# Kernel tuning notes

Measured on AMD Instinct MI355X. Metric: run time of the kernel, lower is better.

Reference implementation:

```python
import jax, jax.numpy as jnp
import numpy as np

THETA = 10000.0
NUM_HEADS = 16


def _rope(x, pos, theta):
    # x: [..., T, d_k], pos: [T]
    d_k = x.shape[-1]
    inv_freq = 1.0 / theta ** (jnp.arange(0, d_k, 2, dtype=jnp.float32) / d_k)
    ang = pos.astype(jnp.float32)[:, None] * inv_freq  # [T, d_k/2]
    cos, sin = jnp.cos(ang), jnp.sin(ang)
    x1, x2 = x[..., ::2], x[..., 1::2]
    even = x1 * cos - x2 * sin
    odd = x1 * sin + x2 * cos
    return jnp.stack([even, odd], axis=-1).reshape(x.shape)


def setup_inputs() -> dict:
    key = jax.random.key(0)
    ks = jax.random.split(key, 5)
    B, T, D = 4, 2048, 1024
    return {
        "in_features": jax.random.normal(ks[0], (B, T, D), dtype=jnp.float32),
        "token_positions": jnp.arange(T, dtype=jnp.int64 if jax.config.jax_enable_x64 else jnp.int32),
        "Wq": jax.random.normal(ks[1], (D, D), dtype=jnp.float32) * 0.02,
        "Wk": jax.random.normal(ks[2], (D, D), dtype=jnp.float32) * 0.02,
        "Wv": jax.random.normal(ks[3], (D, D), dtype=jnp.float32) * 0.02,
        "Wo": jax.random.normal(ks[4], (D, D), dtype=jnp.float32) * 0.02,
    }


def reference(in_features, token_positions, Wq, Wk, Wv, Wo):
    B, T, D = in_features.shape
    h = NUM_HEADS
    d_k = D // h
    # projections (weight stored [out, in], torch applies x @ W.T)
    Q = in_features @ Wq.T
    K = in_features @ Wk.T
    V = in_features @ Wv.T
    # [B, T, h*d_k] -> [B, h, T, d_k]
    Q = Q.reshape(B, T, h, d_k).transpose(0, 2, 1, 3)
    K = K.reshape(B, T, h, d_k).transpose(0, 2, 1, 3)
    V = V.reshape(B, T, h, d_k).transpose(0, 2, 1, 3)
    Q = _rope(Q, token_positions, THETA)
    K = _rope(K, token_positions, THETA)
    scores = jnp.einsum("bhqd,bhkd->bhqk", Q, K) / jnp.sqrt(jnp.float32(d_k))
    causal = jnp.tril(jnp.ones((T, T), dtype=bool))
    scores = jnp.where(causal, scores, -jnp.inf)
    attn = jax.nn.softmax(scores, axis=-1)
    heads = jnp.einsum("bhqk,bhkd->bhqd", attn, V)
    out = heads.transpose(0, 2, 1, 3).reshape(B, T, D)
    return out @ Wo.T
```

## Files before the change

### kernel.cpp

```cpp
#include <hip/hip_runtime.h>


typedef unsigned short u16;
typedef short short8 __attribute__((ext_vector_type(8)));
typedef float f32x4 __attribute__((ext_vector_type(4)));

#if defined(__has_builtin)
#if __has_builtin(__builtin_amdgcn_exp2f)
#define EXP2(x) __builtin_amdgcn_exp2f(x)
#else
#define EXP2(x) exp2f(x)
#endif
#else
#define EXP2(x) exp2f(x)
#endif

#define QSCALE 0.18033688011112042f
#define NEG_L2T_32 -0.4152410118609203f

__device__ __forceinline__ float bf2f(u16 u) {
  return __uint_as_float(((unsigned int)u) << 16);
}
__device__ __forceinline__ u16 f2bf(float f) {
  unsigned int x = __float_as_uint(f);
  x += 0x7fff + ((x >> 16) & 1);
  return (u16)(x >> 16);
}

__device__ __forceinline__ void glds16(const u16* g, u16* l) {
  __builtin_amdgcn_global_load_lds(
      (const __attribute__((address_space(1))) unsigned int*)g,
      (__attribute__((address_space(3))) unsigned int*)l, 16, 0, 0);
}

__global__ __launch_bounds__(256) void cvt_all(
    const float* __restrict__ X, const float* __restrict__ Wq,
    const float* __restrict__ Wk, const float* __restrict__ Wv,
    const float* __restrict__ Wo, u16* __restrict__ Xb,
    u16* __restrict__ Wqkvb, u16* __restrict__ Wob) {
  const int gid = blockIdx.x * 256 + threadIdx.x;
  const int i = gid * 8;
  const int M1 = 1 << 20;
  const float* src;
  u16* dst;
  int off;
  if (i < 8 * M1)        { src = X;  dst = Xb;            off = 0; }
  else if (i < 9 * M1)   { src = Wq; dst = Wqkvb;         off = 8 * M1; }
  else if (i < 10 * M1)  { src = Wk; dst = Wqkvb + M1;    off = 9 * M1; }
  else if (i < 11 * M1)  { src = Wv; dst = Wqkvb + 2*M1;  off = 10 * M1; }
  else                   { src = Wo; dst = Wob;           off = 11 * M1; }
  const int j = i - off;
  const float4 a = *(const float4*)(src + j);
  const float4 b = *(const float4*)(src + j + 4);
  short8 o;
  o[0] = (short)f2bf(a.x); o[1] = (short)f2bf(a.y);
  o[2] = (short)f2bf(a.z); o[3] = (short)f2bf(a.w);
  o[4] = (short)f2bf(b.x); o[5] = (short)f2bf(b.y);
  o[6] = (short)f2bf(b.z); o[7] = (short)f2bf(b.w);
  *(short8*)(dst + j) = o;
}

__global__ __launch_bounds__(256) void gemm_qkv(const u16* __restrict__ A,
                                                const u16* __restrict__ W,
                                                const int* __restrict__ pos,
                                                u16* __restrict__ Qr,
                                                u16* __restrict__ Kr,
                                                u16* __restrict__ Vd) {
  const int K = 1024;
  __shared__ __align__(16) u16 As[128 * 64];
  __shared__ __align__(16) u16 Bs[128 * 64];
  const int tid = threadIdx.x;
  const int m0 = blockIdx.y << 7;
  const int n0 = blockIdx.x << 7;
  const int w = tid >> 6, L = tid & 63;
  const int wm = (w >> 1) << 6, wn = (w & 1) << 6;
  const int lane15 = L & 15, quad = L >> 4;

  f32x4 acc[4][4] = {};

  const u16* Ap[4]; const u16* Bp[4];
  u16* Al[4]; u16* Bl[4];
#pragma unroll
  for (int i = 0; i < 4; ++i) {
    const int s = tid + (i << 8);
    const int row = s >> 3;
    const int c = ((s & 7) ^ (row & 7)) << 3;
    Ap[i] = A + (size_t)(m0 + row) * K + c;
    Bp[i] = W + (size_t)(n0 + row) * K + c;
    Al[i] = &As[s * 8];
    Bl[i] = &Bs[s * 8];
  }

  int offA[4][2], offB[4][2];
#pragma unroll
  for (int mt = 0; mt < 4; ++mt) {
    const int ra = wm + mt * 16 + lane15;
    const int rb = wn + mt * 16 + lane15;
    offA[mt][0] = ra * 64 + ((quad ^ (ra & 7)) << 3);
    offA[mt][1] = ra * 64 + (((quad + 4) ^ (ra & 7)) << 3);
    offB[mt][0] = rb * 64 + ((quad ^ (rb & 7)) << 3);
    offB[mt][1] = rb * 64 + (((quad + 4) ^ (rb & 7)) << 3);
  }

  for (int k0 = 0; k0 < K; k0 += 64) {
    __syncthreads();
#pragma unroll
    for (int i = 0; i < 4; ++i) glds16(Ap[i] + k0, Al[i]);
#pragma unroll
    for (int i = 0; i < 4; ++i) glds16(Bp[i] + k0, Bl[i]);
    __syncthreads();
#pragma unroll
    for (int ks = 0; ks < 2; ++ks) {
      short8 a[4], b[4];
#pragma unroll
      for (int mt = 0; mt < 4; ++mt) a[mt] = *(const short8*)&As[offA[mt][ks]];
#pragma unroll
      for (int nt = 0; nt < 4; ++nt) b[nt] = *(const short8*)&Bs[offB[nt][ks]];
#pragma unroll
      for (int mt = 0; mt < 4; ++mt)
#pragma unroll
        for (int nt = 0; nt < 4; ++nt)
          acc[mt][nt] =
              __builtin_amdgcn_mfma_f32_16x16x32_bf16(a[mt], b[nt], acc[mt][nt], 0, 0, 0);
    }
  }

  const int sel = n0 >> 10;
  const int ncol0 = (n0 & 1023) + wn;
  if (sel == 2) {
#pragma unroll
    for (int mt = 0; mt < 4; ++mt) {
      const int rbase = m0 + wm + mt * 16 + (quad << 2);
#pragma unroll
      for (int nt = 0; nt < 4; ++nt) {
        const int col = ncol0 + nt * 16 + lane15;
#pragma unroll
        for (int r = 0; r < 4; ++r)
          Vd[(size_t)(rbase + r) * 1024 + col] = f2bf(acc[mt][nt][r]);
      }
    }
  } else {
    u16* dst = sel ? Kr : Qr;
    const float sc = sel ? 1.0f : QSCALE;
    float invf[4];
#pragma unroll
    for (int nt = 0; nt < 4; ++nt) {
      const int d2 = ((ncol0 + nt * 16 + lane15) & 63) >> 1;
      invf[nt] = EXP2((float)d2 * NEG_L2T_32);
    }
#pragma unroll
    for (int mt = 0; mt < 4; ++mt) {
      const int rbase = m0 + wm + mt * 16 + (quad << 2);
#pragma unroll
      for (int r = 0; r < 4; ++r) {
        const int m = rbase + r;
        const int bb = m >> 11, tt = m & 2047;
        const float posf = (float)pos[tt];
#pragma unroll
        for (int nt = 0; nt < 4; ++nt) {
          const int col = ncol0 + nt * 16 + lane15;
          const int h = col >> 6, dcol = col & 63;
          float sn, cn;
          __sincosf(posf * invf[nt], &sn, &cn);
          const float self = acc[mt][nt][r];
          const float part = __shfl_xor(self, 1, 64);
          const float res = (dcol & 1) ? (part * sn + self * cn)
                                       : (self * cn - part * sn);
          dst[(((size_t)((bb * 16 + h) * 2048 + tt)) << 6) + dcol] = f2bf(res * sc);
        }
      }
    }
  }
}

__global__ __launch_bounds__(256) void gemm_bt(const u16* __restrict__ A,
                                               const u16* __restrict__ B,
                                               float* __restrict__ C,
                                               int M, int N, int K) {
  __shared__ __align__(16) u16 As[64 * 32];
  __shared__ __align__(16) u16 Bs[128 * 32];
  const int tid = threadIdx.x;
  const int m0 = blockIdx.y << 6;
  const int n0 = blockIdx.x << 7;
  const int w = tid >> 6, L = tid & 63;
  const int wm = (w >> 1) << 5, wn = (w & 1) << 6;
  const int lane15 = L & 15, quad = L >> 4;
  const int koff = quad << 3;

  f32x4 acc[2][4] = {};

  const int s0 = tid, s1 = tid + 256;
  const u16* A0 = A + (size_t)(m0 + (s0 >> 2)) * K + ((s0 & 3) << 3);
  const u16* B0 = B + (size_t)(n0 + (s0 >> 2)) * K + ((s0 & 3) << 3);
  const u16* B1 = B + (size_t)(n0 + (s1 >> 2)) * K + ((s1 & 3) << 3);
  u16* asd0 = &As[s0 * 8];
  u16* bsd0 = &Bs[s0 * 8]; u16* bsd1 = &Bs[s1 * 8];

  for (int k0 = 0; k0 < K; k0 += 32) {
    __syncthreads();
    glds16(A0 + k0, asd0);
    glds16(B0 + k0, bsd0);
    glds16(B1 + k0, bsd1);
    __syncthreads();
    short8 a[2], b[4];
#pragma unroll
    for (int mt = 0; mt < 2; ++mt)
      a[mt] = *(const short8*)&As[(wm + mt * 16 + lane15) * 32 + koff];
#pragma unroll
    for (int nt = 0; nt < 4; ++nt)
      b[nt] = *(const short8*)&Bs[(wn + nt * 16 + lane15) * 32 + koff];
#pragma unroll
    for (int mt = 0; mt < 2; ++mt)
#pragma unroll
      for (int nt = 0; nt < 4; ++nt)
        acc[mt][nt] =
            __builtin_amdgcn_mfma_f32_16x16x32_bf16(a[mt], b[nt], acc[mt][nt], 0, 0, 0);
  }

#pragma unroll
  for (int mt = 0; mt < 2; ++mt) {
    const int rbase = m0 + wm + mt * 16 + (quad << 2);
#pragma unroll
    for (int nt = 0; nt < 4; ++nt) {
      const int col = n0 + wn + nt * 16 + lane15;
#pragma unroll
      for (int r = 0; r < 4; ++r)
        C[(size_t)(rbase + r) * N + col] = acc[mt][nt][r];
    }
  }
}

__global__ __launch_bounds__(256) void transpose_v(const u16* __restrict__ Vlin,
                                                   u16* __restrict__ Vt) {
  __shared__ __align__(16) u16 tile[64][68];
  const int tid = threadIdx.x;
  const int bh = blockIdx.y, b = bh >> 4, h = bh & 15;
  const int t0 = blockIdx.x << 6;
#pragma unroll
  for (int i = 0; i < 4; ++i) {
    int s = tid + (i << 8);
    int tl = s >> 4, c4 = (s & 15) << 2;
    *(uint2*)&tile[tl][c4] =
        *(const uint2*)(Vlin + (((size_t)(b * 2048 + t0 + tl)) << 10) + (h << 6) + c4);
  }
  __syncthreads();
#pragma unroll
  for (int i = 0; i < 4; ++i) {
    int s = tid + (i << 8);
    int d = s >> 4, t4 = (s & 15) << 2;
    uint2 o;
    o.x = (unsigned)tile[t4 + 0][d] | ((unsigned)tile[t4 + 1][d] << 16);
    o.y = (unsigned)tile[t4 + 2][d] | ((unsigned)tile[t4 + 3][d] << 16);
    *(uint2*)(Vt + (((size_t)(bh * 64 + d)) << 11) + t0 + t4) = o;
  }
}

__global__ __launch_bounds__(256) void flash_attn(const u16* __restrict__ Q,
                                                  const u16* __restrict__ Kk,
                                                  const u16* __restrict__ Vt,
                                                  u16* __restrict__ O) {
  __shared__ __align__(16) u16 Ksm[64 * 72];
  __shared__ __align__(16) u16 Vsm[64 * 72];
  __shared__ __align__(16) u16 Psm[8][16 * 64];
  const int tid = threadIdx.x;
  const int w = tid >> 6, L = tid & 63;
  const int lane15 = L & 15, quad = L >> 4;
  const int g = blockIdx.x >> 6;
  const int bh = blockIdx.x & 63;
  const int b = bh >> 4, h = bh & 15;
  const int rq = lane15 >> 2;

  const int s0 = tid, s1 = tid + 256;
  const u16* kbase = Kk + ((size_t)bh << 17);
  const u16* kp0 = kbase + s0 * 8;
  const u16* kp1 = kbase + s1 * 8;
  const u16* vbase = Vt + ((size_t)bh << 17);
  const u16* vp0 = vbase + (size_t)(s0 >> 3) * 2048 + (s0 & 7) * 8;
  const u16* vp1 = vbase + (size_t)(s1 >> 3) * 2048 + (s1 & 7) * 8;
  const int d0 = (s0 >> 3) * 72 + (s0 & 7) * 8;
  const int d1 = (s1 >> 3) * 72 + (s1 & 7) * 8;

  for (int pass = 0; pass < 2; ++pass) {
    const int qt = pass ? (15 - g) : g;
    const int nkt = 2 * qt + 2;

    const size_t qrow = (size_t)bh * 2048 + qt * 128 + w * 32;
    short8 qa[2][2];
#pragma unroll
    for (int hf = 0; hf < 2; ++hf) {
      const size_t qb = (qrow + hf * 16 + lane15) << 6;
      qa[hf][0] = *(const short8*)(Q + qb + (quad << 3));
      qa[hf][1] = *(const short8*)(Q + qb + 32 + (quad << 3));
    }

    uint4 kr0 = *(const uint4*)kp0;
    uint4 kr1 = *(const uint4*)kp1;
    uint4 vr0 = *(const uint4*)vp0;
    uint4 vr1 = *(const uint4*)vp1;
    __syncthreads();
    *(uint4*)&Ksm[d0] = kr0; *(uint4*)&Ksm[d1] = kr1;
    *(uint4*)&Vsm[d0] = vr0; *(uint4*)&Vsm[d1] = vr1;
    __syncthreads();

    f32x4 o_acc[2][4] = {};
    float l_part[2][4] = {};
    const int B0w = qt * 128 + w * 32;

    for (int kt = 0; kt < nkt; ++kt) {
      if (kt + 1 < nkt) {
        kr0 = *(const uint4*)(kp0 + (size_t)(kt + 1) * 4096);
        kr1 = *(const uint4*)(kp1 + (size_t)(kt + 1) * 4096);
        vr0 = *(const uint4*)(vp0 + (kt + 1) * 64);
        vr1 = *(const uint4*)(vp1 + (kt + 1) * 64);
      }

      short8 kb[4][2];
#pragma unroll
      for (int nt = 0; nt < 4; ++nt) {
        kb[nt][0] = *(const short8*)&Ksm[(nt * 16 + lane15) * 72 + (quad << 3)];
        kb[nt][1] = *(const short8*)&Ksm[(nt * 16 + lane15) * 72 + 32 + (quad << 3)];
      }

      const bool act0 = (kt * 64 <= B0w + 15);
      const bool act1 = (kt * 64 <= B0w + 31);

#pragma unroll
      for (int hf = 0; hf < 2; ++hf) {
        const int B0 = B0w + hf * 16;
        if (kt * 64 > B0 + 15) continue;
        u16* pw = Psm[w * 2 + hf];

        f32x4 sc[4];
#pragma unroll
        for (int nt = 0; nt < 4; ++nt) {
          f32x4 a = {};
          a = __builtin_amdgcn_mfma_f32_16x16x32_bf16(qa[hf][0], kb[nt][0], a, 0, 0, 0);
          a = __builtin_amdgcn_mfma_f32_16x16x32_bf16(qa[hf][1], kb[nt][1], a, 0, 0, 0);
          sc[nt] = a;
        }

        if (kt * 64 + 63 > B0) {
#pragma unroll
          for (int nt = 0; nt < 4; ++nt)
#pragma unroll
            for (int r = 0; r < 4; ++r) {
              const int row = B0 + (quad << 2) + r;
              const int key = kt * 64 + nt * 16 + lane15;
              if (key > row) sc[nt][r] = -1e30f;
            }
        }

#pragma unroll
        for (int nt = 0; nt < 4; ++nt) {
          const int colsw = ((nt ^ quad) << 4) + lane15;
#pragma unroll
          for (int r = 0; r < 4; ++r) {
            const float p = EXP2(sc[nt][r]);
            l_part[hf][r] += p;
            pw[((quad << 2) + r) * 64 + colsw] = (u16)(__float_as_uint(p) >> 16);
          }
        }
      }
      asm volatile("" ::: "memory");

      short8 pa[2][2];
      if (act0) {
#pragma unroll
        for (int ks = 0; ks < 2; ++ks)
          pa[0][ks] = *(const short8*)&Psm[w * 2][lane15 * 64 +
                                               ((ks * 32 + quad * 8) ^ (rq << 4))];
      }
      if (act1) {
#pragma unroll
        for (int ks = 0; ks < 2; ++ks)
          pa[1][ks] = *(const short8*)&Psm[w * 2 + 1][lane15 * 64 +
                                               ((ks * 32 + quad * 8) ^ (rq << 4))];
      }
#pragma unroll
      for (int ks = 0; ks < 2; ++ks) {
#pragma unroll
        for (int dt = 0; dt < 4; ++dt) {
          const short8 vb =
              *(const short8*)&Vsm[(dt * 16 + lane15) * 72 + ks * 32 + quad * 8];
          if (act0)
            o_acc[0][dt] =
                __builtin_amdgcn_mfma_f32_16x16x32_bf16(pa[0][ks], vb, o_acc[0][dt], 0, 0, 0);
          if (act1)
            o_acc[1][dt] =
                __builtin_amdgcn_mfma_f32_16x16x32_bf16(pa[1][ks], vb, o_acc[1][dt], 0, 0, 0);
        }
      }

      if (kt + 1 < nkt) {
        __syncthreads();
        *(uint4*)&Ksm[d0] = kr0; *(uint4*)&Ksm[d1] = kr1;
        *(uint4*)&Vsm[d0] = vr0; *(uint4*)&Vsm[d1] = vr1;
        __syncthreads();
      }
    }

#pragma unroll
    for (int hf = 0; hf < 2; ++hf) {
#pragma unroll
      for (int r = 0; r < 4; ++r) {
        float l = l_part[hf][r];
#pragma unroll
        for (int off = 1; off < 16; off <<= 1) l += __shfl_xor(l, off, 64);
        const float inv = 1.f / l;
        const int t = qt * 128 + w * 32 + hf * 16 + (quad << 2) + r;
        const size_t obase = (((size_t)b * 2048 + t) << 10) + (h << 6);
#pragma unroll
        for (int dt = 0; dt < 4; ++dt)
          O[obase + dt * 16 + lane15] = f2bf(o_acc[hf][dt][r] * inv);
      }
    }
  }
}

extern "C" void kernel_launch(void* const* d_in, const int* in_sizes, int n_in,
                              void* d_out, int out_size, void* d_ws, size_t ws_size,
                              hipStream_t stream) {
  const float* X  = (const float*)d_in[0];
  const int* pos  = (const int*)d_in[1];
  const float* Wq = (const float*)d_in[2];
  const float* Wk = (const float*)d_in[3];
  const float* Wv = (const float*)d_in[4];
  const float* Wo = (const float*)d_in[5];
  float* out = (float*)d_out;

  char* ws = (char*)d_ws;
  const size_t SZ = (size_t)8192 * 1024 * sizeof(u16);
  const size_t WSZ = (size_t)1024 * 1024 * sizeof(u16);
  u16* Vlin = (u16*)(ws + 0 * SZ);
  u16* Qr   = (u16*)(ws + 1 * SZ);
  u16* Kr   = (u16*)(ws + 2 * SZ);
  u16* Vt   = (u16*)(ws + 3 * SZ);
  u16* Xb   = (u16*)(ws + 4 * SZ);
  u16* Oh   = Vlin;
  char* wtail = ws + 5 * SZ;
  u16* Wqkvb = (u16*)(wtail);
  u16* Wob   = (u16*)(wtail + 3 * WSZ);

  const dim3 blk(256);

  cvt_all<<<6144, blk, 0, stream>>>(X, Wq, Wk, Wv, Wo, Xb, Wqkvb, Wob);
  gemm_qkv<<<dim3(24, 64), blk, 0, stream>>>(Xb, Wqkvb, pos, Qr, Kr, Vlin);
  transpose_v<<<dim3(32, 64), blk, 0, stream>>>(Vlin, Vt);
  flash_attn<<<512, blk, 0, stream>>>(Qr, Kr, Vt, Oh);
  gemm_bt<<<dim3(8, 128), blk, 0, stream>>>(Oh, Wob, out, 8192, 1024, 1024);
}
```

Before: 271.4 us.

## Fuse V transpose into QKV GEMM, double-buffer attention K/V, widen output GEMM K-tile

The QKV GEMM epilogue for V tiles now stages the accumulator through shared memory with a swizzle and writes V directly in transposed [b,h,d,t] layout, so the separate transpose kernel and its round trip through global memory go away. Flash attention double-buffers its K/V shared tiles, which drops one barrier per iteration. The output projection GEMM moves to a 64-wide K tile with XOR-swizzled LDS addressing, halving the number of loop iterations and barriers. The cost is more shared memory per block, which may lower occupancy, plus an extra sync in the QKV epilogue.

```diff
diff --git a/kernel.cpp b/kernel.cpp
--- a/kernel.cpp
+++ b/kernel.cpp
@@ -25,6 +25,9 @@
   unsigned int x = __float_as_uint(f);
   x += 0x7fff + ((x >> 16) & 1);
   return (u16)(x >> 16);
+}
+__device__ __forceinline__ unsigned int pack2(float x, float y) {
+  return (unsigned int)f2bf(x) | ((unsigned int)f2bf(y) << 16);
 }
 
 __device__ __forceinline__ void glds16(const u16* g, u16* l) {
@@ -65,10 +68,11 @@
                                                 const int* __restrict__ pos,
                                                 u16* __restrict__ Qr,
                                                 u16* __restrict__ Kr,
-                                                u16* __restrict__ Vd) {
+                                                u16* __restrict__ Vt) {
   const int K = 1024;
-  __shared__ __align__(16) u16 As[128 * 64];
-  __shared__ __align__(16) u16 Bs[128 * 64];
+  __shared__ __align__(16) u16 SM[16384];
+  u16* As = SM;
+  u16* Bs = SM + 8192;
   const int tid = threadIdx.x;
   const int m0 = blockIdx.y << 7;
   const int n0 = blockIdx.x << 7;
@@ -126,18 +130,34 @@
   }
 
   const int sel = n0 >> 10;
-  const int ncol0 = (n0 & 1023) + wn;
+  const int ncol0w = (n0 & 1023) + wn;
   if (sel == 2) {
+    const int b = m0 >> 11, t0 = m0 & 2047;
+    const int h0 = (n0 & 1023) >> 6;
+    __syncthreads();
 #pragma unroll
     for (int mt = 0; mt < 4; ++mt) {
-      const int rbase = m0 + wm + mt * 16 + (quad << 2);
+      const int tb = wm + mt * 16 + (quad << 2);
 #pragma unroll
       for (int nt = 0; nt < 4; ++nt) {
-        const int col = ncol0 + nt * 16 + lane15;
-#pragma unroll
-        for (int r = 0; r < 4; ++r)
-          Vd[(size_t)(rbase + r) * 1024 + col] = f2bf(acc[mt][nt][r]);
-      }
+        const int dp = wn + nt * 16 + lane15;
+        const int e = dp * 128 + ((tb & ~7) ^ ((dp & 15) << 3)) + (tb & 7);
+        uint2 v;
+        v.x = pack2(acc[mt][nt][0], acc[mt][nt][1]);
+        v.y = pack2(acc[mt][nt][2], acc[mt][nt][3]);
+        *(uint2*)&SM[e] = v;
+      }
+    }
+    __syncthreads();
+    const int chunk = tid & 15;
+#pragma unroll
+    for (int i = 0; i < 8; ++i) {
+      const int dp = (tid >> 4) + (i << 4);
+      const int e = dp * 128 + ((chunk << 3) ^ ((dp & 15) << 3));
+      const uint4 v = *(const uint4*)&SM[e];
+      const int bh = b * 16 + h0 + (dp >> 6);
+      const int d = dp & 63;
+      *(uint4*)(Vt + (((size_t)(bh * 64 + d)) << 11) + t0 + (chunk << 3)) = v;
     }
   } else {
     u16* dst = sel ? Kr : Qr;
@@ -145,7 +165,7 @@
     float invf[4];
 #pragma unroll
     for (int nt = 0; nt < 4; ++nt) {
-      const int d2 = ((ncol0 + nt * 16 + lane15) & 63) >> 1;
+      const int d2 = ((ncol0w + nt * 16 + lane15) & 63) >> 1;
       invf[nt] = EXP2((float)d2 * NEG_L2T_32);
     }
 #pragma unroll
@@ -158,7 +178,7 @@
         const float posf = (float)pos[tt];
 #pragma unroll
         for (int nt = 0; nt < 4; ++nt) {
-          const int col = ncol0 + nt * 16 + lane15;
+          const int col = ncol0w + nt * 16 + lane15;
           const int h = col >> 6, dcol = col & 63;
           float sn, cn;
           __sincosf(posf * invf[nt], &sn, &cn);
@@ -177,44 +197,71 @@
                                                const u16* __restrict__ B,
                                                float* __restrict__ C,
                                                int M, int N, int K) {
-  __shared__ __align__(16) u16 As[64 * 32];
-  __shared__ __align__(16) u16 Bs[128 * 32];
+  __shared__ __align__(16) u16 As[64 * 64];
+  __shared__ __align__(16) u16 Bs[128 * 64];
   const int tid = threadIdx.x;
   const int m0 = blockIdx.y << 6;
   const int n0 = blockIdx.x << 7;
   const int w = tid >> 6, L = tid & 63;
   const int wm = (w >> 1) << 5, wn = (w & 1) << 6;
   const int lane15 = L & 15, quad = L >> 4;
-  const int koff = quad << 3;
 
   f32x4 acc[2][4] = {};
 
-  const int s0 = tid, s1 = tid + 256;
-  const u16* A0 = A + (size_t)(m0 + (s0 >> 2)) * K + ((s0 & 3) << 3);
-  const u16* B0 = B + (size_t)(n0 + (s0 >> 2)) * K + ((s0 & 3) << 3);
-  const u16* B1 = B + (size_t)(n0 + (s1 >> 2)) * K + ((s1 & 3) << 3);
-  u16* asd0 = &As[s0 * 8];
-  u16* bsd0 = &Bs[s0 * 8]; u16* bsd1 = &Bs[s1 * 8];
-
-  for (int k0 = 0; k0 < K; k0 += 32) {
-    __syncthreads();
-    glds16(A0 + k0, asd0);
-    glds16(B0 + k0, bsd0);
-    glds16(B1 + k0, bsd1);
-    __syncthreads();
-    short8 a[2], b[4];
-#pragma unroll
-    for (int mt = 0; mt < 2; ++mt)
-      a[mt] = *(const short8*)&As[(wm + mt * 16 + lane15) * 32 + koff];
-#pragma unroll
-    for (int nt = 0; nt < 4; ++nt)
-      b[nt] = *(const short8*)&Bs[(wn + nt * 16 + lane15) * 32 + koff];
-#pragma unroll
-    for (int mt = 0; mt < 2; ++mt)
-#pragma unroll
-      for (int nt = 0; nt < 4; ++nt)
-        acc[mt][nt] =
-            __builtin_amdgcn_mfma_f32_16x16x32_bf16(a[mt], b[nt], acc[mt][nt], 0, 0, 0);
+  const u16* Ap[2]; const u16* Bp[4];
+  u16* Al[2]; u16* Bl[4];
+#pragma unroll
+  for (int i = 0; i < 2; ++i) {
+    const int s = tid + (i << 8);
+    const int row = s >> 3;
+    const int c = ((s & 7) ^ (row & 7)) << 3;
+    Ap[i] = A + (size_t)(m0 + row) * K + c;
+    Al[i] = &As[s * 8];
+  }
+#pragma unroll
+  for (int i = 0; i < 4; ++i) {
+    const int s = tid + (i << 8);
+    const int row = s >> 3;
+    const int c = ((s & 7) ^ (row & 7)) << 3;
+    Bp[i] = B + (size_t)(n0 + row) * K + c;
+    Bl[i] = &Bs[s * 8];
+  }
+
+  int offA[2][2], offB[4][2];
+#pragma unroll
+  for (int mt = 0; mt < 2; ++mt) {
+    const int ra = wm + mt * 16 + lane15;
+    offA[mt][0] = ra * 64 + ((quad ^ (ra & 7)) << 3);
+    offA[mt][1] = ra * 64 + (((quad + 4) ^ (ra & 7)) << 3);
+  }
+#pragma unroll
+  for (int nt = 0; nt < 4; ++nt) {
+    const int rb = wn + nt * 16 + lane15;
+    offB[nt][0] = rb * 64 + ((quad ^ (rb & 7)) << 3);
+    offB[nt][1] = rb * 64 + (((quad + 4) ^ (rb & 7)) << 3);
+  }
+
+  for (int k0 = 0; k0 < K; k0 += 64) {
+    __syncthreads();
+#pragma unroll
+    for (int i = 0; i < 2; ++i) glds16(Ap[i] + k0, Al[i]);
+#pragma unroll
+    for (int i = 0; i < 4; ++i) glds16(Bp[i] + k0, Bl[i]);
+    __syncthreads();
+#pragma unroll
+    for (int ks = 0; ks < 2; ++ks) {
+      short8 a[2], b[4];
+#pragma unroll
+      for (int mt = 0; mt < 2; ++mt) a[mt] = *(const short8*)&As[offA[mt][ks]];
+#pragma unroll
+      for (int nt = 0; nt < 4; ++nt) b[nt] = *(const short8*)&Bs[offB[nt][ks]];
+#pragma unroll
+      for (int mt = 0; mt < 2; ++mt)
+#pragma unroll
+        for (int nt = 0; nt < 4; ++nt)
+          acc[mt][nt] =
+              __builtin_amdgcn_mfma_f32_16x16x32_bf16(a[mt], b[nt], acc[mt][nt], 0, 0, 0);
+    }
   }
 
 #pragma unroll
@@ -227,31 +274,6 @@
       for (int r = 0; r < 4; ++r)
         C[(size_t)(rbase + r) * N + col] = acc[mt][nt][r];
     }
-  }
-}
-
-__global__ __launch_bounds__(256) void transpose_v(const u16* __restrict__ Vlin,
-                                                   u16* __restrict__ Vt) {
-  __shared__ __align__(16) u16 tile[64][68];
-  const int tid = threadIdx.x;
-  const int bh = blockIdx.y, b = bh >> 4, h = bh & 15;
-  const int t0 = blockIdx.x << 6;
-#pragma unroll
-  for (int i = 0; i < 4; ++i) {
-    int s = tid + (i << 8);
-    int tl = s >> 4, c4 = (s & 15) << 2;
-    *(uint2*)&tile[tl][c4] =
-        *(const uint2*)(Vlin + (((size_t)(b * 2048 + t0 + tl)) << 10) + (h << 6) + c4);
-  }
-  __syncthreads();
-#pragma unroll
-  for (int i = 0; i < 4; ++i) {
-    int s = tid + (i << 8);
-    int d = s >> 4, t4 = (s & 15) << 2;
-    uint2 o;
-    o.x = (unsigned)tile[t4 + 0][d] | ((unsigned)tile[t4 + 1][d] << 16);
-    o.y = (unsigned)tile[t4 + 2][d] | ((unsigned)tile[t4 + 3][d] << 16);
-    *(uint2*)(Vt + (((size_t)(bh * 64 + d)) << 11) + t0 + t4) = o;
   }
 }
 
@@ -259,8 +281,8 @@
                                                   const u16* __restrict__ Kk,
                                                   const u16* __restrict__ Vt,
                                                   u16* __restrict__ O) {
-  __shared__ __align__(16) u16 Ksm[64 * 72];
-  __shared__ __align__(16) u16 Vsm[64 * 72];
+  __shared__ __align__(16) u16 Ksm[2][64 * 72];
+  __shared__ __align__(16) u16 Vsm[2][64 * 72];
   __shared__ __align__(16) u16 Psm[8][16 * 64];
   const int tid = threadIdx.x;
   const int w = tid >> 6, L = tid & 63;
@@ -297,9 +319,8 @@
     uint4 kr1 = *(const uint4*)kp1;
     uint4 vr0 = *(const uint4*)vp0;
     uint4 vr1 = *(const uint4*)vp1;
-    __syncthreads();
-    *(uint4*)&Ksm[d0] = kr0; *(uint4*)&Ksm[d1] = kr1;
-    *(uint4*)&Vsm[d0] = vr0; *(uint4*)&Vsm[d1] = vr1;
+    *(uint4*)&Ksm[0][d0] = kr0; *(uint4*)&Ksm[0][d1] = kr1;
+    *(uint4*)&Vsm[0][d0] = vr0; *(uint4*)&Vsm[0][d1] = vr1;
     __syncthreads();
 
     f32x4 o_acc[2][4] = {};
@@ -307,18 +328,21 @@
     const int B0w = qt * 128 + w * 32;
 
     for (int kt = 0; kt < nkt; ++kt) {
+      const int cur = kt & 1, nxt = cur ^ 1;
       if (kt + 1 < nkt) {
         kr0 = *(const uint4*)(kp0 + (size_t)(kt + 1) * 4096);
         kr1 = *(const uint4*)(kp1 + (size_t)(kt + 1) * 4096);
         vr0 = *(const uint4*)(vp0 + (kt + 1) * 64);
         vr1 = *(const uint4*)(vp1 + (kt + 1) * 64);
       }
+      const u16* Ks = Ksm[cur];
+      const u16* Vs = Vsm[cur];
 
       short8 kb[4][2];
 #pragma unroll
       for (int nt = 0; nt < 4; ++nt) {
-        kb[nt][0] = *(const short8*)&Ksm[(nt * 16 + lane15) * 72 + (quad << 3)];
-        kb[nt][1] = *(const short8*)&Ksm[(nt * 16 + lane15) * 72 + 32 + (quad << 3)];
+        kb[nt][0] = *(const short8*)&Ks[(nt * 16 + lane15) * 72 + (quad << 3)];
+        kb[nt][1] = *(const short8*)&Ks[(nt * 16 + lane15) * 72 + 32 + (quad << 3)];
       }
 
       const bool act0 = (kt * 64 <= B0w + 15);
@@ -381,7 +405,7 @@
 #pragma unroll
         for (int dt = 0; dt < 4; ++dt) {
           const short8 vb =
-              *(const short8*)&Vsm[(dt * 16 + lane15) * 72 + ks * 32 + quad * 8];
+              *(const short8*)&Vs[(dt * 16 + lane15) * 72 + ks * 32 + quad * 8];
           if (act0)
             o_acc[0][dt] =
                 __builtin_amdgcn_mfma_f32_16x16x32_bf16(pa[0][ks], vb, o_acc[0][dt], 0, 0, 0);
@@ -392,9 +416,8 @@
       }
 
       if (kt + 1 < nkt) {
-        __syncthreads();
-        *(uint4*)&Ksm[d0] = kr0; *(uint4*)&Ksm[d1] = kr1;
-        *(uint4*)&Vsm[d0] = vr0; *(uint4*)&Vsm[d1] = vr1;
+        *(uint4*)&Ksm[nxt][d0] = kr0; *(uint4*)&Ksm[nxt][d1] = kr1;
+        *(uint4*)&Vsm[nxt][d0] = vr0; *(uint4*)&Vsm[nxt][d1] = vr1;
         __syncthreads();
       }
     }
@@ -431,12 +454,11 @@
   char* ws = (char*)d_ws;
   const size_t SZ = (size_t)8192 * 1024 * sizeof(u16);
   const size_t WSZ = (size_t)1024 * 1024 * sizeof(u16);
-  u16* Vlin = (u16*)(ws + 0 * SZ);
+  u16* Vt   = (u16*)(ws + 0 * SZ);
   u16* Qr   = (u16*)(ws + 1 * SZ);
   u16* Kr   = (u16*)(ws + 2 * SZ);
-  u16* Vt   = (u16*)(ws + 3 * SZ);
-  u16* Xb   = (u16*)(ws + 4 * SZ);
-  u16* Oh   = Vlin;
+  u16* Xb   = (u16*)(ws + 3 * SZ);
+  u16* Oh   = (u16*)(ws + 4 * SZ);
   char* wtail = ws + 5 * SZ;
   u16* Wqkvb = (u16*)(wtail);
   u16* Wob   = (u16*)(wtail + 3 * WSZ);
@@ -444,8 +466,7 @@
   const dim3 blk(256);
 
   cvt_all<<<6144, blk, 0, stream>>>(X, Wq, Wk, Wv, Wo, Xb, Wqkvb, Wob);
-  gemm_qkv<<<dim3(24, 64), blk, 0, stream>>>(Xb, Wqkvb, pos, Qr, Kr, Vlin);
-  transpose_v<<<dim3(32, 64), blk, 0, stream>>>(Vlin, Vt);
+  gemm_qkv<<<dim3(24, 64), blk, 0, stream>>>(Xb, Wqkvb, pos, Qr, Kr, Vt);
   flash_attn<<<512, blk, 0, stream>>>(Qr, Kr, Vt, Oh);
   gemm_bt<<<dim3(8, 128), blk, 0, stream>>>(Oh, Wob, out, 8192, 1024, 1024);
 }
```

New measurement: 260.1 us. -4.2%, faster.
